# Performance work log

Measured on AMD Instinct MI355X. Metric: run time of the kernel, lower is better.

Reference implementation:

```python
import jax, jax.numpy as jnp
import numpy as np

B, C, H, W = 4, 3, 32, 32
N_IMAGES = 32
TIMESTEPS = 20


def _extract_patches(x, pad_mode):
    """3x3 patches at every spatial location. x: [B,C,H,W] -> [B,C,9,H,W]."""
    if pad_mode == 'wrap':
        xp = jnp.pad(x, ((0, 0), (0, 0), (1, 1), (1, 1)), mode='wrap')
    else:
        xp = jnp.pad(x, ((0, 0), (0, 0), (1, 1), (1, 1)))
    h, w = x.shape[2], x.shape[3]
    sl = [xp[:, :, di:di + h, dj:dj + w] for di in range(3) for dj in range(3)]
    return jnp.stack(sl, axis=2)  # [B,C,9,H,W], k = di*3+dj (torch unfold order)


def setup_inputs() -> dict:
    key = jax.random.key(0)
    k1, k2 = jax.random.split(key)
    x = jax.random.normal(k1, (B, C, H, W), dtype=jnp.float32)
    images = jax.random.uniform(k2, (N_IMAGES, C, H, W), dtype=jnp.float32)
    # linear beta schedule, as in _noise_buffers
    betas = jnp.linspace(1e-4, 0.02, TIMESTEPS, dtype=jnp.float32)
    alpha_cumprod = jnp.cumprod(1.0 - betas)
    mu_sched = jnp.sqrt(alpha_cumprod)
    sigma_sched = jnp.sqrt(1.0 - alpha_cumprod)
    return {"x": x, "images": images, "mu_sched": mu_sched,
            "sigma_sched": sigma_sched, "t": 10}


def reference(x, images, mu_sched, sigma_sched, t):
    mu = mu_sched[t]
    sigma = sigma_sched[t]
    b, c, h, w = x.shape

    # x-side: circular-padded 3x3 patches and their squared norms
    xp = _extract_patches(x, 'wrap').reshape(b, c * 9, h, w)   # [B,C*9,H,W]
    x_norms = jnp.sum(xp * xp, axis=1)                          # [B,H,W]

    # dataset-side: zero-padded 3x3 patches at every pixel of every image
    ip = _extract_patches(images, 'zeros')                      # [N,C,9,H,W]
    patches = ip.transpose(0, 3, 4, 1, 2).reshape(-1, c * 9)    # [P, C*9], P=N*H*W
    pnorms = jnp.sum(patches * patches, axis=1)                 # [P]
    pcenters = patches.reshape(-1, c, 9)[:, :, 4]               # [P,C] center pixel (1,1)

    # conv2d(x_pad, patches) == contraction over the C*9 patch axis
    conv = jnp.einsum('bkhw,pk->bphw', xp, patches)             # [B,P,H,W]

    inv2s2 = 1.0 / (2.0 * sigma * sigma)
    log_w = -(x_norms[:, None] - 2.0 * mu * conv
              + (mu * mu) * pnorms[None, :, None, None]) * inv2s2  # [B,P,H,W]

    # stable softmax-style weights over the patch axis (== online LSE result)
    m = jnp.max(log_w, axis=1)                                  # [B,H,W]
    wgt = jnp.exp(log_w - m[:, None])                           # [B,P,H,W]
    sum_w = jnp.sum(wgt, axis=1)                                # [B,H,W]

    # sum_p w * (x - mu * pcenter) = x*sum_w - mu * (w @ pcenters)
    wc = jnp.einsum('bphw,pc->bchw', wgt, pcenters)             # [B,C,H,W]
    sum_wd = x * sum_w[:, None] - mu * wc
    return -sum_wd / (sigma * sigma * sum_w[:, None])
```

## Files before the change

kernel.cpp:

```cpp
#include <hip/hip_runtime.h>
#include <cstddef>

#define P_TOTAL 32768
#define Q_TOTAL 4096
#define NSPLIT 128
#define KPS 256
#define TILES 16
#define NGROUP 8
#define QPERWG 256
#define NQG (Q_TOTAL / QPERWG)
#define GRID (NSPLIT * NQG)

#define KEYS_B 16384
#define VT_OFF KEYS_B
#define VT_PITCH 528
#define LDS_TOTAL (VT_OFF + 4 * VT_PITCH)

typedef _Float16 half8 __attribute__((ext_vector_type(8)));
typedef __fp16 fp16x2 __attribute__((ext_vector_type(2)));
typedef __fp16 fp16x4 __attribute__((ext_vector_type(4)));
typedef __fp16 fp16x8 __attribute__((ext_vector_type(8)));
typedef float floatx4 __attribute__((ext_vector_type(4)));

union h8cast { fp16x8 a; half8 b; };

__device__ __forceinline__ float fexp2(float x) {
#if defined(__has_builtin) && __has_builtin(__builtin_amdgcn_exp2f)
    return __builtin_amdgcn_exp2f(x);
#else
    return exp2f(x);
#endif
}

__global__ __launch_bounds__(256) void qbuild_k(
    const float* __restrict__ x, _Float16* __restrict__ q16)
{
    int q = blockIdx.x * 256 + threadIdx.x;
    int b = q >> 10, rem = q & 1023, h = rem >> 5, w = rem & 31;
    const float* xb = x + (size_t)b * 3072;
    _Float16 row[32];
    #pragma unroll
    for (int c = 0; c < 3; c++)
      #pragma unroll
      for (int di = 0; di < 3; di++)
        #pragma unroll
        for (int dj = 0; dj < 3; dj++)
            row[c * 9 + di * 3 + dj] =
                (_Float16)xb[c * 1024 + ((h + di + 31) & 31) * 32 + ((w + dj + 31) & 31)];
    row[27] = (_Float16)1.0f;
    row[28] = (_Float16)0.f; row[29] = (_Float16)0.f;
    row[30] = (_Float16)0.f; row[31] = (_Float16)0.f;
    _Float16* qp = q16 + (size_t)q * 32;
    #pragma unroll
    for (int u = 0; u < 4; u++) ((float4*)qp)[u] = ((float4*)row)[u];
}

__global__ __launch_bounds__(256) void score_k(
    const _Float16* __restrict__ q16, const float* __restrict__ images,
    const float* __restrict__ mu_sched, const float* __restrict__ sigma_sched,
    const int* __restrict__ tptr, float* __restrict__ partials)
{
    __shared__ char lds[LDS_TOTAL];
    int tid = threadIdx.x;
    int split = blockIdx.x >> 4;
    int qg    = blockIdx.x & 15;

    int t = tptr[0];
    float mu = mu_sched[t], sg = sigma_sched[t];
    const float LOG2E = 1.4426950408889634f;
    float inv2s2 = 1.0f / (2.0f * sg * sg);
    float s1     = 2.0f * mu * inv2s2 * LOG2E;
    float bscale = -mu * mu * inv2s2 * LOG2E;

    {
        int r = tid;
        int m16 = r & 15, tt = (r >> 4) & 1, tp = r >> 5;
        int kk = tp * 32 + (m16 >> 2) * 8 + tt * 4 + (m16 & 3);
        int p = split * KPS + kk;
        int n = p >> 10, rem = p & 1023, i = rem >> 5, j = rem & 31;
        const float* img = images + (size_t)n * 3072;
        _Float16 hrow[32];
        float pnorm = 0.f, c0 = 0.f, c1 = 0.f, c2 = 0.f;
        #pragma unroll
        for (int c = 0; c < 3; c++)
          #pragma unroll
          for (int di = 0; di < 3; di++)
            #pragma unroll
            for (int dj = 0; dj < 3; dj++) {
                int ii = i + di - 1, jj = j + dj - 1;
                float val = 0.f;
                if (ii >= 0 && ii < 32 && jj >= 0 && jj < 32)
                    val = img[c * 1024 + ii * 32 + jj];
                hrow[c * 9 + di * 3 + dj] = (_Float16)(val * s1);
                pnorm = fmaf(val, val, pnorm);
                if (di == 1 && dj == 1) { if (c == 0) c0 = val; else if (c == 1) c1 = val; else c2 = val; }
            }
        hrow[27] = (_Float16)(pnorm * bscale);
        hrow[28] = (_Float16)0.f; hrow[29] = (_Float16)0.f;
        hrow[30] = (_Float16)0.f; hrow[31] = (_Float16)0.f;
        int sw = (r >> 1) & 3;
        float4* src4 = (float4*)hrow;
        #pragma unroll
        for (int c = 0; c < 4; c++)
            *(float4*)(lds + r * 64 + ((c ^ sw) << 4)) = src4[c];
        _Float16* vt = (_Float16*)(lds + VT_OFF);
        vt[0 * (VT_PITCH / 2) + kk] = (_Float16)1.0f;
        vt[1 * (VT_PITCH / 2) + kk] = (_Float16)c0;
        vt[2 * (VT_PITCH / 2) + kk] = (_Float16)c1;
        vt[3 * (VT_PITCH / 2) + kk] = (_Float16)c2;
    }

    int lane = tid & 63, wid = tid >> 6;
    int col  = lane & 15, quad = lane >> 4;
    int qbase = qg * QPERWG + wid * 64;

    half8 qf[4];
    #pragma unroll
    for (int f = 0; f < 4; f++)
        qf[f] = *(const half8*)(q16 + (size_t)(qbase + f * 16 + col) * 32 + quad * 8);
    __syncthreads();

    int swc = (col >> 1) & 3;
    const char* abase = lds + col * 64 + ((quad ^ swc) << 4);

    float mx[4];
    {
        floatx4 mv[4];
        #pragma unroll
        for (int f = 0; f < 4; f++) mv[f] = (floatx4){-3e38f, -3e38f, -3e38f, -3e38f};
        #pragma unroll 4
        for (int tile = 0; tile < TILES; tile++) {
            half8 ak = *(const half8*)(abase + tile * 1024);
            #pragma unroll
            for (int f = 0; f < 4; f++) {
                floatx4 a = __builtin_amdgcn_mfma_f32_16x16x32_f16(
                    ak, qf[f], (floatx4){0.f, 0.f, 0.f, 0.f}, 0, 0, 0);
                mv[f] = __builtin_elementwise_max(mv[f], a);
            }
        }
        #pragma unroll
        for (int f = 0; f < 4; f++) {
            mx[f] = fmaxf(fmaxf(mv[f][0], mv[f][1]), fmaxf(mv[f][2], mv[f][3]));
            mx[f] = fmaxf(mx[f], __shfl_xor(mx[f], 16, 64));
            mx[f] = fmaxf(mx[f], __shfl_xor(mx[f], 32, 64));
        }
    }
    floatx4 nmv[4];
    #pragma unroll
    for (int f = 0; f < 4; f++)
        nmv[f] = (floatx4){-mx[f], -mx[f], -mx[f], -mx[f]};

    if (quad == 0) {
        #pragma unroll
        for (int f = 0; f < 4; f++)
            partials[(size_t)split * Q_TOTAL + qbase + f * 16 + col] = mx[f];
    }

    const char* vrow = lds + VT_OFF + col * VT_PITCH;
    floatx4 acc[4];
    #pragma unroll
    for (int f = 0; f < 4; f++) acc[f] = (floatx4){0.f, 0.f, 0.f, 0.f};

    #pragma unroll 2
    for (int g = 0; g < NGROUP; g++) {
        half8 ak0 = *(const half8*)(abase + (2 * g) * 1024);
        half8 ak1 = *(const half8*)(abase + (2 * g + 1) * 1024);
        half8 av = (half8)(_Float16)0.f;
        if (col < 4) av = *(const half8*)(vrow + g * 64 + quad * 16);
        #pragma unroll
        for (int f = 0; f < 4; f++) {
            floatx4 a0 = __builtin_amdgcn_mfma_f32_16x16x32_f16(ak0, qf[f], nmv[f], 0, 0, 0);
            floatx4 a1 = __builtin_amdgcn_mfma_f32_16x16x32_f16(ak1, qf[f], nmv[f], 0, 0, 0);
            fp16x2 p00 = __builtin_amdgcn_cvt_pkrtz(fexp2(a0[0]), fexp2(a0[1]));
            fp16x2 p01 = __builtin_amdgcn_cvt_pkrtz(fexp2(a0[2]), fexp2(a0[3]));
            fp16x2 p10 = __builtin_amdgcn_cvt_pkrtz(fexp2(a1[0]), fexp2(a1[1]));
            fp16x2 p11 = __builtin_amdgcn_cvt_pkrtz(fexp2(a1[2]), fexp2(a1[3]));
            fp16x4 lo = __builtin_shufflevector(p00, p01, 0, 1, 2, 3);
            fp16x4 hi = __builtin_shufflevector(p10, p11, 0, 1, 2, 3);
            h8cast u; u.a = __builtin_shufflevector(lo, hi, 0, 1, 2, 3, 4, 5, 6, 7);
            acc[f] = __builtin_amdgcn_mfma_f32_16x16x32_f16(av, u.b, acc[f], 0, 0, 0);
        }
    }

    if (quad == 0) {
        const size_t PL = (size_t)NSPLIT * Q_TOTAL;
        #pragma unroll
        for (int f = 0; f < 4; f++) {
            size_t idx = (size_t)split * Q_TOTAL + qbase + f * 16 + col;
            partials[idx + PL]     = acc[f][0];
            partials[idx + PL * 2] = acc[f][1];
            partials[idx + PL * 3] = acc[f][2];
            partials[idx + PL * 4] = acc[f][3];
        }
    }
}

__global__ __launch_bounds__(256) void combine_k(
    const float* __restrict__ x, const float* __restrict__ partials,
    const float* __restrict__ mu_sched, const float* __restrict__ sigma_sched,
    const int* __restrict__ tptr, float* __restrict__ out)
{
    __shared__ float red[5][4][64];
    int tid = threadIdx.x;
    int wid = tid >> 6, lane = tid & 63;
    int q = blockIdx.x * 64 + lane;
    int t = tptr[0];
    float mu = mu_sched[t], sg = sigma_sched[t];
    float inv_s2 = 1.0f / (sg * sg);

    const size_t PL = (size_t)NSPLIT * Q_TOTAL;
    float M = -3e38f, S = 0.f, W0 = 0.f, W1 = 0.f, W2 = 0.f;
    int sp0 = wid * (NSPLIT / 4);
    #pragma unroll 4
    for (int i = 0; i < NSPLIT / 4; i++) {
        size_t idx = (size_t)(sp0 + i) * Q_TOTAL + q;
        float mval = partials[idx];
        float mnew = fmaxf(M, mval);
        float sco = fexp2(M - mnew), scn = fexp2(mval - mnew);
        S  = fmaf(S,  sco, partials[idx + PL] * scn);
        W0 = fmaf(W0, sco, partials[idx + PL * 2] * scn);
        W1 = fmaf(W1, sco, partials[idx + PL * 3] * scn);
        W2 = fmaf(W2, sco, partials[idx + PL * 4] * scn);
        M = mnew;
    }
    red[0][wid][lane] = M;  red[1][wid][lane] = S;
    red[2][wid][lane] = W0; red[3][wid][lane] = W1; red[4][wid][lane] = W2;
    __syncthreads();

    if (wid == 0) {
        float Mf = red[0][0][lane];
        #pragma unroll
        for (int wv = 1; wv < 4; wv++) Mf = fmaxf(Mf, red[0][wv][lane]);
        float Sf = 0.f, A = 0.f, B = 0.f, C = 0.f;
        #pragma unroll
        for (int wv = 0; wv < 4; wv++) {
            float r = fexp2(red[0][wv][lane] - Mf);
            Sf = fmaf(red[1][wv][lane], r, Sf);
            A  = fmaf(red[2][wv][lane], r, A);
            B  = fmaf(red[3][wv][lane], r, B);
            C  = fmaf(red[4][wv][lane], r, C);
        }
        float invS = 1.0f / Sf;
        int b = q >> 10, rem = q & 1023;
        #pragma unroll
        for (int c = 0; c < 3; c++) {
            float Wc = (c == 0) ? A : (c == 1 ? B : C);
            float xc = x[(size_t)b * 3072 + c * 1024 + rem];
            out[(size_t)b * 3072 + c * 1024 + rem] = -(xc - mu * Wc * invS) * inv_s2;
        }
    }
}

extern "C" void kernel_launch(void* const* d_in, const int* in_sizes, int n_in,
                              void* d_out, int out_size, void* d_ws, size_t ws_size,
                              hipStream_t stream) {
    const float* x      = (const float*)d_in[0];
    const float* images = (const float*)d_in[1];
    const float* mu_s   = (const float*)d_in[2];
    const float* sg_s   = (const float*)d_in[3];
    const int*   tptr   = (const int*)d_in[4];
    float* out = (float*)d_out;

    float*    partials = (float*)d_ws;
    _Float16* q16      = (_Float16*)((char*)d_ws + (size_t)5 * NSPLIT * Q_TOTAL * 4);

    qbuild_k<<<Q_TOTAL / 256, 256, 0, stream>>>(x, q16);
    score_k<<<GRID, 256, 0, stream>>>(q16, images, mu_s, sg_s, tptr, partials);
    combine_k<<<Q_TOTAL / 64, 256, 0, stream>>>(
        x, partials, mu_s, sg_s, tptr, out);
}
```

Before: 100.4 us.

## Fuse combine pass into score kernel using a ticket-based last-blocks finisher

Merges the separate combine kernel into the score kernel: each block increments a global ticket after writing partials, and the last 64 blocks to arrive wait for all blocks to finish and then perform the split-merge and output for 64 queries each. This removes a kernel launch and its inter-kernel gap, but adds a memset of the ticket and a spin-wait that serializes the finishing work on only 64 blocks. It relies on those blocks being resident while the others complete.

```diff
diff --git a/kernel.cpp b/kernel.cpp
--- a/kernel.cpp
+++ b/kernel.cpp
@@ -10,6 +10,7 @@
 #define QPERWG 256
 #define NQG (Q_TOTAL / QPERWG)
 #define GRID (NSPLIT * NQG)
+#define FINW 64
 
 #define KEYS_B 16384
 #define VT_OFF KEYS_B
@@ -55,12 +56,15 @@
     for (int u = 0; u < 4; u++) ((float4*)qp)[u] = ((float4*)row)[u];
 }
 
-__global__ __launch_bounds__(256) void score_k(
-    const _Float16* __restrict__ q16, const float* __restrict__ images,
+__global__ __launch_bounds__(256) void score2_k(
+    const _Float16* __restrict__ q16, const float* __restrict__ x,
+    const float* __restrict__ images,
     const float* __restrict__ mu_sched, const float* __restrict__ sigma_sched,
-    const int* __restrict__ tptr, float* __restrict__ partials)
+    const int* __restrict__ tptr, float* __restrict__ partials,
+    int* __restrict__ ticket, float* __restrict__ out)
 {
     __shared__ char lds[LDS_TOTAL];
+    __shared__ int ticket_s;
     int tid = threadIdx.x;
     int split = blockIdx.x >> 4;
     int qg    = blockIdx.x & 15;
@@ -71,6 +75,7 @@
     float inv2s2 = 1.0f / (2.0f * sg * sg);
     float s1     = 2.0f * mu * inv2s2 * LOG2E;
     float bscale = -mu * mu * inv2s2 * LOG2E;
+    float inv_s2 = 1.0f / (sg * sg);
 
     {
         int r = tid;
@@ -193,20 +198,24 @@
             partials[idx + PL * 4] = acc[f][3];
         }
     }
-}
-
-__global__ __launch_bounds__(256) void combine_k(
-    const float* __restrict__ x, const float* __restrict__ partials,
-    const float* __restrict__ mu_sched, const float* __restrict__ sigma_sched,
-    const int* __restrict__ tptr, float* __restrict__ out)
-{
-    __shared__ float red[5][4][64];
-    int tid = threadIdx.x;
-    int wid = tid >> 6, lane = tid & 63;
-    int q = blockIdx.x * 64 + lane;
-    int t = tptr[0];
-    float mu = mu_sched[t], sg = sigma_sched[t];
-    float inv_s2 = 1.0f / (sg * sg);
+
+    __threadfence();
+    __syncthreads();
+    if (tid == 0) ticket_s = atomicAdd(ticket, 1);
+    __syncthreads();
+    int old = ticket_s;
+    if (old < GRID - FINW) return;
+
+    if (tid == 0) {
+        while (__hip_atomic_load(ticket, __ATOMIC_RELAXED, __HIP_MEMORY_SCOPE_AGENT) < GRID)
+            __builtin_amdgcn_s_sleep(2);
+    }
+    __syncthreads();
+    __threadfence();
+
+    int fid = old - (GRID - FINW);
+    int q = fid * 64 + lane;
+    float* red = (float*)lds;
 
     const size_t PL = (size_t)NSPLIT * Q_TOTAL;
     float M = -3e38f, S = 0.f, W0 = 0.f, W1 = 0.f, W2 = 0.f;
@@ -223,22 +232,26 @@
         W2 = fmaf(W2, sco, partials[idx + PL * 4] * scn);
         M = mnew;
     }
-    red[0][wid][lane] = M;  red[1][wid][lane] = S;
-    red[2][wid][lane] = W0; red[3][wid][lane] = W1; red[4][wid][lane] = W2;
+    red[(0 * 4 + wid) * 64 + lane] = M;
+    red[(1 * 4 + wid) * 64 + lane] = S;
+    red[(2 * 4 + wid) * 64 + lane] = W0;
+    red[(3 * 4 + wid) * 64 + lane] = W1;
+    red[(4 * 4 + wid) * 64 + lane] = W2;
     __syncthreads();
 
     if (wid == 0) {
-        float Mf = red[0][0][lane];
-        #pragma unroll
-        for (int wv = 1; wv < 4; wv++) Mf = fmaxf(Mf, red[0][wv][lane]);
+        float Mf = red[(0 * 4 + 0) * 64 + lane];
+        #pragma unroll
+        for (int wv = 1; wv < 4; wv++)
+            Mf = fmaxf(Mf, red[(0 * 4 + wv) * 64 + lane]);
         float Sf = 0.f, A = 0.f, B = 0.f, C = 0.f;
         #pragma unroll
         for (int wv = 0; wv < 4; wv++) {
-            float r = fexp2(red[0][wv][lane] - Mf);
-            Sf = fmaf(red[1][wv][lane], r, Sf);
-            A  = fmaf(red[2][wv][lane], r, A);
-            B  = fmaf(red[3][wv][lane], r, B);
-            C  = fmaf(red[4][wv][lane], r, C);
+            float r = fexp2(red[(0 * 4 + wv) * 64 + lane] - Mf);
+            Sf = fmaf(red[(1 * 4 + wv) * 64 + lane], r, Sf);
+            A  = fmaf(red[(2 * 4 + wv) * 64 + lane], r, A);
+            B  = fmaf(red[(3 * 4 + wv) * 64 + lane], r, B);
+            C  = fmaf(red[(4 * 4 + wv) * 64 + lane], r, C);
         }
         float invS = 1.0f / Sf;
         int b = q >> 10, rem = q & 1023;
@@ -263,9 +276,10 @@
 
     float*    partials = (float*)d_ws;
     _Float16* q16      = (_Float16*)((char*)d_ws + (size_t)5 * NSPLIT * Q_TOTAL * 4);
-
+    int*      ticket   = (int*)((char*)q16 + (size_t)Q_TOTAL * 32 * 2);
+
+    hipMemsetAsync(ticket, 0, 4, stream);
     qbuild_k<<<Q_TOTAL / 256, 256, 0, stream>>>(x, q16);
-    score_k<<<GRID, 256, 0, stream>>>(q16, images, mu_s, sg_s, tptr, partials);
-    combine_k<<<Q_TOTAL / 64, 256, 0, stream>>>(
-        x, partials, mu_s, sg_s, tptr, out);
-}
+    score2_k<<<GRID, 256, 0, stream>>>(
+        q16, x, images, mu_s, sg_s, tptr, partials, ticket, out);
+}
```

Result: slower. 307.3 us (+206.0%).
